# Kernel tuning notes

Measured on AMD Instinct MI355X. Metric: run time of the kernel, lower is better.

## Reference

```python
import jax, jax.numpy as jnp
import numpy as np

D, M, K, L, H, BS = 128, 8, 256, 2, 256, 1024


def setup_inputs() -> dict:
    key = jax.random.key(0)
    ks = jax.random.split(key, 7)
    s_d = 1.0 / np.sqrt(D)
    s_2d = 1.0 / np.sqrt(2 * D)
    s_h = 1.0 / np.sqrt(H)
    x = jax.random.normal(ks[0], (BS, D), jnp.float32)
    codebook0 = jax.random.uniform(ks[1], (K, D), jnp.float32, -s_d, s_d)
    codebooks = jax.random.uniform(ks[2], (M - 1, K, D), jnp.float32, -s_d, s_d)
    Wc = jax.random.uniform(ks[3], (M - 1, D, 2 * D), jnp.float32, -s_2d, s_2d)
    bc = jax.random.uniform(ks[4], (M - 1, D), jnp.float32, -s_2d, s_2d)
    W1 = jax.random.uniform(ks[5], (M - 1, L, H, D), jnp.float32, -s_d, s_d)
    W2 = jax.random.uniform(ks[6], (M - 1, L, D, H), jnp.float32, -s_h, s_h)
    return {"x": x, "codebook0": codebook0, "codebooks": codebooks,
            "Wc": Wc, "bc": bc, "W1": W1, "W2": W2}


def _step_targets(xhat, cb, Wc_m, bc_m, W1_m, W2_m):
    """Candidate quantization targets for one step. xhat:[bs,d], cb:[K,d] -> [bs,K,d].
    MLPconcat(concat(zqs, xhat)) is split into the zqs part and the xhat part so the
    [bs*K, 2d] repeat of the torch code is never materialized (same math)."""
    Wz, Wx = Wc_m[:, :D], Wc_m[:, D:]          # Linear(2d,d): y = cc @ W.T + b
    z = cb[None, :, :] + (cb @ Wz.T)[None, :, :] + (xhat @ Wx.T)[:, None, :] + bc_m  # [bs,K,d]
    for l in range(L):
        z = z + jnp.maximum(jnp.einsum('bkd,hd->bkh', z, W1_m[l]), 0.0) @ W2_m[l].T
    return z + xhat[:, None, :]


def _encode(x, codebook0, codebooks, Wc, bc, W1, W2):
    # step 0: plain nearest-centroid assignment (assign_to_codebook)
    d0 = (x * x).sum(-1, keepdims=True) + (codebook0 * codebook0).sum(-1) - 2.0 * x @ codebook0.T
    code0 = jnp.argmin(d0, axis=1)
    xhat = codebook0[code0]
    codes = [code0]
    xn = (x * x).sum(-1, keepdims=True)        # [bs,1]
    for m in range(M - 1):
        z = _step_targets(xhat, codebooks[m], Wc[m], bc[m], W1[m], W2[m])  # [bs,K,d]
        dist = xn + (z * z).sum(-1) - 2.0 * jnp.einsum('bd,bkd->bk', x, z)
        idx = jnp.argmin(dist, axis=1)
        xhat = jnp.take_along_axis(z, idx[:, None, None], axis=1)[:, 0, :]
        codes.append(idx)
    return jnp.stack(codes, axis=1)            # [bs, M] int


def _decode(codes, codebook0, codebooks, Wc, bc, W1, W2):
    xhat = codebook0[codes[:, 0]]
    side = [xhat]
    for m in range(M - 1):
        zq = codebooks[m][codes[:, m + 1]]     # [bs,d]
        Wz, Wx = Wc[m][:, :D], Wc[m][:, D:]
        z = zq + zq @ Wz.T + xhat @ Wx.T + bc[m]
        for l in range(L):
            z = z + jnp.maximum(z @ W1[m, l].T, 0.0) @ W2[m, l].T
        xhat = xhat + z
        side.append(xhat)
    return xhat, side


def reference(x, codebook0, codebooks, Wc, bc, W1, W2):
    # forward(): encode under no_grad, then differentiable decode with side outputs
    codes = jax.lax.stop_gradient(_encode(x, codebook0, codebooks, Wc, bc, W1, W2))
    xhat, side = _decode(codes, codebook0, codebooks, Wc, bc, W1, W2)
    return (xhat, codes, tuple(side))
```

## Files before the change

kernel.cpp:

```cpp
#include <hip/hip_runtime.h>


typedef _Float16 f16;
typedef f16 half4_t __attribute__((ext_vector_type(4)));
typedef f16 half8_t __attribute__((ext_vector_type(8)));
typedef float f32x16 __attribute__((ext_vector_type(16)));

#define OUT_CODES 131072
#define OUT_SIDE  139264

#define WS_XHAT  0
#define WS_RB    131072
#define WS_Y     262144
#define WS_ZC    393216
#define WS_BESTD 425984
#define WS_BESTI 430080
#define WS_BESTZ 434176
#define WS_WSPLIT 960000
#define NW1 458752

#define HLO 8192

__device__ __forceinline__ f32x16 mfma_f16(half8_t a, half8_t b, f32x16 c) {
  return __builtin_amdgcn_mfma_f32_32x32x16_f16(a, b, c, 0, 0, 0);
}

__global__ __launch_bounds__(256) void k_wsplit(const float* __restrict__ W1,
    const float* __restrict__ W2, f16* __restrict__ wsh)
{
  int i = (blockIdx.x * 256 + threadIdx.x) * 4;
  const float* src;
  f16* hi;
  if (i < NW1) { src = W1 + i; hi = wsh + i; }
  else         { src = W2 + (i - NW1); hi = wsh + 2 * NW1 + (i - NW1); }
  f16* lo = hi + NW1;
  float4 v = *(const float4*)src;
  half4_t h, l;
  float s;
  s = v.x * 256.f; h[0] = (f16)s; l[0] = (f16)(s - (float)h[0]);
  s = v.y * 256.f; h[1] = (f16)s; l[1] = (f16)(s - (float)h[1]);
  s = v.z * 256.f; h[2] = (f16)s; l[2] = (f16)(s - (float)h[2]);
  s = v.w * 256.f; h[3] = (f16)s; l[3] = (f16)(s - (float)h[3]);
  *(half4_t*)hi = h;
  *(half4_t*)lo = l;
}

__global__ __launch_bounds__(256) void k_step0(const float* __restrict__ x,
    const float* __restrict__ cb0, float* __restrict__ ws, float* __restrict__ out)
{
  __shared__ float xs[128];
  __shared__ float redv[4];
  __shared__ int   redi[4];
  __shared__ int   kwin;
  int tx = threadIdx.x, b = blockIdx.x;
  if (tx < 128) xs[tx] = x[b * 128 + tx];
  __syncthreads();
  const float* c = cb0 + tx * 128;
  float s = 0.f;
  for (int d = 0; d < 128; d += 4) {
    float4 cv = *(const float4*)(c + d);
    float4 xv = *(const float4*)(xs + d);
    float a0 = xv.x - cv.x, a1 = xv.y - cv.y, a2 = xv.z - cv.z, a3 = xv.w - cv.w;
    s += a0 * a0 + a1 * a1 + a2 * a2 + a3 * a3;
  }
  float v = s; int idx = tx;
  for (int off = 32; off; off >>= 1) {
    float v2 = __shfl_xor(v, off);
    int   i2 = __shfl_xor(idx, off);
    if (v2 < v || (v2 == v && i2 < idx)) { v = v2; idx = i2; }
  }
  if ((tx & 63) == 0) { redv[tx >> 6] = v; redi[tx >> 6] = idx; }
  __syncthreads();
  if (tx == 0) {
    float bv = redv[0]; int bi = redi[0];
    for (int w = 1; w < 4; w++)
      if (redv[w] < bv || (redv[w] == bv && redi[w] < bi)) { bv = redv[w]; bi = redi[w]; }
    kwin = bi;
    out[OUT_CODES + b * 8] = (float)bi;
  }
  __syncthreads();
  int k = kwin;
  if (tx < 128) {
    float xh = cb0[k * 128 + tx];
    ws[WS_XHAT + b * 128 + tx] = xh;
    ws[WS_RB   + b * 128 + tx] = xs[tx] - xh;
    out[OUT_SIDE + b * 128 + tx] = xh;
  }
}

__global__ __launch_bounds__(128) void k_prep(const float* __restrict__ cb,
    const float* __restrict__ Wc, const float* __restrict__ bcm, float* __restrict__ ws)
{
  __shared__ float row[128];
  int tx = threadIdx.x, blk = blockIdx.x;
  if (blk < 256) {
    row[tx] = cb[blk * 128 + tx];
    __syncthreads();
    const float* wrow = Wc + tx * 256;
    float s = 0.f;
    for (int d = 0; d < 128; d += 4) {
      float4 wv = *(const float4*)(wrow + d);
      float4 zv = *(const float4*)(row + d);
      s += wv.x * zv.x + wv.y * zv.y + wv.z * zv.z + wv.w * zv.w;
    }
    ws[WS_ZC + blk * 128 + tx] = row[tx] + s + bcm[tx];
  } else {
    int b = blk - 256;
    row[tx] = ws[WS_XHAT + b * 128 + tx];
    __syncthreads();
    const float* wrow = Wc + tx * 256 + 128;
    float s = 0.f;
    for (int d = 0; d < 128; d += 4) {
      float4 wv = *(const float4*)(wrow + d);
      float4 zv = *(const float4*)(row + d);
      s += wv.x * zv.x + wv.y * zv.y + wv.z * zv.z + wv.w * zv.w;
    }
    ws[WS_Y + b * 128 + tx] = s;
  }
}

__global__ __launch_bounds__(256, 2) void k_step(const f16* __restrict__ wsh,
    float* __restrict__ ws, int sm)
{
  __shared__ __align__(16) f16 lds[32768];
  f16* Zh = lds;
  f16* Zl = lds + HLO;
  f16* Hh = lds + 2 * HLO;
  f16* Hl = lds + 3 * HLO;
  int tx = threadIdx.x;
  int lane = tx & 63, w = tx >> 6;
  int col = lane & 31, koct = lane >> 5;
  int b = blockIdx.x >> 2, t = blockIdx.x & 3, k0 = t << 6;

  {
    const float* zc = ws + WS_ZC + k0 * 128;
    const float* y  = ws + WS_Y + b * 128;
    for (int idx = tx; idx < 1024; idx += 256) {
      int m = idx & 63, d0 = (idx >> 6) << 3;
      float4 a  = *(const float4*)(zc + m * 128 + d0);
      float4 bb = *(const float4*)(zc + m * 128 + d0 + 4);
      float4 ya = *(const float4*)(y + d0);
      float4 yb = *(const float4*)(y + d0 + 4);
      float sv[8] = {a.x + ya.x, a.y + ya.y, a.z + ya.z, a.w + ya.w,
                     bb.x + yb.x, bb.y + yb.y, bb.z + yb.z, bb.w + yb.w};
      half8_t h8, l8;
#pragma unroll
      for (int j = 0; j < 8; j++) {
        float v = sv[j] * 256.f;
        f16 h = (f16)v; h8[j] = h; l8[j] = (f16)(v - (float)h);
      }
      int c0 = (d0 + ((m & 15) << 3)) & 127;
      *(half8_t*)(Zh + (m << 7) + c0) = h8;
      *(half8_t*)(Zl + (m << 7) + c0) = l8;
    }
  }
  __syncthreads();

  const int rot0 = (col & 15) << 3;
  const f16* Zr0 = Zh + (col << 7);
  const f16* Zr1 = Zh + ((col + 32) << 7);
  const f16* Hr0 = Hh + (col << 7);
  const f16* Hr1 = Hh + ((col + 32) << 7);

  for (int l = 0; l < 2; l++) {
    const f16* w1h = wsh + (size_t)((sm * 2 + l) * 256) * 128;
    const f16* w2h = wsh + 2 * NW1 + (size_t)((sm * 2 + l) * 128) * 256;
    f32x16 acc2[2];
#pragma unroll
    for (int i = 0; i < 16; i++) { acc2[0][i] = 0.f; acc2[1][i] = 0.f; }

#pragma unroll
    for (int hf = 0; hf < 2; hf++) {
      const f16* a1p = w1h + (size_t)((hf << 7) + (w << 5) + col) * 128 + (koct << 3);
      const f16* a2p = w2h + (size_t)((w << 5) + col) * 256 + (hf << 7) + (koct << 3);
      half8_t a1hv[8], a1lv[8], a2hv[8], a2lv[8];
#pragma unroll
      for (int kc = 0; kc < 8; kc++) {
        a1hv[kc] = *(const half8_t*)(a1p + (kc << 4));
        a1lv[kc] = *(const half8_t*)(a1p + NW1 + (kc << 4));
      }
#pragma unroll
      for (int kc = 0; kc < 8; kc++) {
        a2hv[kc] = *(const half8_t*)(a2p + (kc << 4));
        a2lv[kc] = *(const half8_t*)(a2p + NW1 + (kc << 4));
      }

      f32x16 acc1[2];
#pragma unroll
      for (int i = 0; i < 16; i++) { acc1[0][i] = 0.f; acc1[1][i] = 0.f; }
#pragma unroll
      for (int kc = 0; kc < 8; kc++) {
        int poff = (((kc << 4) + (koct << 3)) + rot0) & 127;
        half8_t bh0 = *(const half8_t*)(Zr0 + poff);
        half8_t bl0 = *(const half8_t*)(Zr0 + HLO + poff);
        half8_t bh1 = *(const half8_t*)(Zr1 + poff);
        half8_t bl1 = *(const half8_t*)(Zr1 + HLO + poff);
        acc1[0] = mfma_f16(a1hv[kc], bh0, acc1[0]);
        acc1[1] = mfma_f16(a1hv[kc], bh1, acc1[1]);
        acc1[0] = mfma_f16(a1lv[kc], bh0, acc1[0]);
        acc1[1] = mfma_f16(a1lv[kc], bh1, acc1[1]);
        acc1[0] = mfma_f16(a1hv[kc], bl0, acc1[0]);
        acc1[1] = mfma_f16(a1hv[kc], bl1, acc1[1]);
      }
#pragma unroll
      for (int mt = 0; mt < 2; mt++) {
        int m = (mt << 5) + col;
#pragma unroll
        for (int qd = 0; qd < 4; qd++) {
          half4_t hv, lv;
#pragma unroll
          for (int j = 0; j < 4; j++) {
            float tv = fmaxf(acc1[mt][(qd << 2) + j], 0.f) * 0.00390625f;
            f16 h = (f16)tv; hv[j] = h; lv[j] = (f16)(tv - (float)h);
          }
          int c = (((w << 5) + (qd << 3) + (koct << 2)) + rot0) & 127;
          *(half4_t*)(Hh + (m << 7) + c) = hv;
          *(half4_t*)(Hl + (m << 7) + c) = lv;
        }
      }
      __syncthreads();
#pragma unroll
      for (int kc = 0; kc < 8; kc++) {
        int poff = (((kc << 4) + (koct << 3)) + rot0) & 127;
        half8_t bh0 = *(const half8_t*)(Hr0 + poff);
        half8_t bl0 = *(const half8_t*)(Hr0 + HLO + poff);
        half8_t bh1 = *(const half8_t*)(Hr1 + poff);
        half8_t bl1 = *(const half8_t*)(Hr1 + HLO + poff);
        acc2[0] = mfma_f16(a2hv[kc], bh0, acc2[0]);
        acc2[1] = mfma_f16(a2hv[kc], bh1, acc2[1]);
        acc2[0] = mfma_f16(a2lv[kc], bh0, acc2[0]);
        acc2[1] = mfma_f16(a2lv[kc], bh1, acc2[1]);
        acc2[0] = mfma_f16(a2hv[kc], bl0, acc2[0]);
        acc2[1] = mfma_f16(a2hv[kc], bl1, acc2[1]);
      }
      __syncthreads();
    }
#pragma unroll
    for (int mt = 0; mt < 2; mt++) {
      int m = (mt << 5) + col;
      f16* zhr = Zh + (m << 7);
      f16* zlr = Zl + (m << 7);
#pragma unroll
      for (int qd = 0; qd < 4; qd++) {
        int c = (((w << 5) + (qd << 3) + (koct << 2)) + rot0) & 127;
        half4_t zh = *(half4_t*)(zhr + c);
        half4_t zl = *(half4_t*)(zlr + c);
#pragma unroll
        for (int j = 0; j < 4; j++) {
          float zs = (float)zh[j] + (float)zl[j];
          zs += acc2[mt][(qd << 2) + j] * 0.00390625f;
          f16 h = (f16)zs; zh[j] = h; zl[j] = (f16)(zs - (float)h);
        }
        *(half4_t*)(zhr + c) = zh;
        *(half4_t*)(zlr + c) = zl;
      }
    }
    __syncthreads();
  }

  float* pd = (float*)Hh;
  int* rwin = (int*)Hh + 64;
  {
    int row = tx >> 2, seg = tx & 3;
    int rotr = (row & 15) << 3;
    const f16* zhr = Zh + (row << 7);
    const f16* zlr = Zl + (row << 7);
    const float* rb = ws + WS_RB + b * 128 + (seg << 5);
    float s = 0.f;
#pragma unroll
    for (int o = 0; o < 4; o++) {
      int c = (((seg << 5) + (o << 3)) + rotr) & 127;
      half8_t zh = *(const half8_t*)(zhr + c);
      half8_t zl = *(const half8_t*)(zlr + c);
      float4 r0 = *(const float4*)(rb + (o << 3));
      float4 r1 = *(const float4*)(rb + (o << 3) + 4);
      float rr[8] = {r0.x, r0.y, r0.z, r0.w, r1.x, r1.y, r1.z, r1.w};
#pragma unroll
      for (int j = 0; j < 8; j++) {
        float z = ((float)zh[j] + (float)zl[j]) * 0.00390625f;
        float dlt = rr[j] - z;
        s += dlt * dlt;
      }
    }
    s += __shfl_xor(s, 1);
    s += __shfl_xor(s, 2);
    if (seg == 0) pd[row] = s;
  }
  __syncthreads();
  if (tx < 64) {
    float v = pd[tx]; int idx = tx;
#pragma unroll
    for (int off = 32; off; off >>= 1) {
      float v2 = __shfl_xor(v, off);
      int   i2 = __shfl_xor(idx, off);
      if (v2 < v || (v2 == v && i2 < idx)) { v = v2; idx = i2; }
    }
    if (tx == 0) {
      ws[WS_BESTD + (b << 2) + t] = v;
      ((int*)ws)[WS_BESTI + (b << 2) + t] = k0 + idx;
      rwin[0] = idx;
    }
  }
  __syncthreads();
  if (tx < 32) {
    int rw = rwin[0];
    int c = ((tx << 2) + ((rw & 15) << 3)) & 127;
    half4_t zh = *(const half4_t*)(Zh + (rw << 7) + c);
    half4_t zl = *(const half4_t*)(Zl + (rw << 7) + c);
    float4 z;
    z.x = ((float)zh[0] + (float)zl[0]) * 0.00390625f;
    z.y = ((float)zh[1] + (float)zl[1]) * 0.00390625f;
    z.z = ((float)zh[2] + (float)zl[2]) * 0.00390625f;
    z.w = ((float)zh[3] + (float)zl[3]) * 0.00390625f;
    *(float4*)(ws + WS_BESTZ + (((b << 2) + t) << 7) + (tx << 2)) = z;
  }
}

__global__ __launch_bounds__(128) void k_update(const float* __restrict__ x,
    float* __restrict__ ws, float* __restrict__ out, int m, int last)
{
  __shared__ int tsel;
  int tx = threadIdx.x, b = blockIdx.x;
  if (tx == 0) {
    float bv = ws[WS_BESTD + (b << 2)]; int bt = 0;
    for (int q = 1; q < 4; q++) {
      float v = ws[WS_BESTD + (b << 2) + q];
      if (v < bv) { bv = v; bt = q; }
    }
    tsel = bt;
    int k = ((const int*)ws)[WS_BESTI + (b << 2) + bt];
    out[OUT_CODES + b * 8 + (m + 1)] = (float)k;
  }
  __syncthreads();
  int bt = tsel;
  float z  = ws[WS_BESTZ + (((b << 2) + bt) << 7) + tx];
  float xh = ws[WS_XHAT + b * 128 + tx] + z;
  ws[WS_XHAT + b * 128 + tx] = xh;
  ws[WS_RB   + b * 128 + tx] = x[b * 128 + tx] - xh;
  out[OUT_SIDE + (m + 1) * 131072 + b * 128 + tx] = xh;
  if (last) out[b * 128 + tx] = xh;
}

extern "C" void kernel_launch(void* const* d_in, const int* in_sizes, int n_in,
                              void* d_out, int out_size, void* d_ws, size_t ws_size,
                              hipStream_t stream)
{
  const float* x   = (const float*)d_in[0];
  const float* cb0 = (const float*)d_in[1];
  const float* cbs = (const float*)d_in[2];
  const float* Wc  = (const float*)d_in[3];
  const float* bc  = (const float*)d_in[4];
  const float* W1  = (const float*)d_in[5];
  const float* W2  = (const float*)d_in[6];
  float* out = (float*)d_out;
  float* ws  = (float*)d_ws;
  f16* wsh = (f16*)(ws + WS_WSPLIT);

  k_wsplit<<<896, 256, 0, stream>>>(W1, W2, wsh);
  k_step0<<<1024, 256, 0, stream>>>(x, cb0, ws, out);
  for (int m = 0; m < 7; m++) {
    k_prep<<<1280, 128, 0, stream>>>(cbs + m * 256 * 128, Wc + m * 128 * 256,
                                     bc + m * 128, ws);
    k_step<<<4096, 256, 0, stream>>>(wsh, ws, m);
    k_update<<<1024, 128, 0, stream>>>(x, ws, out, m, (m == 6) ? 1 : 0);
  }
}
```

Baseline: 2.138 ms.

## Retile MFMA warps to 2x2 grid with split-K accumulators for ILP

Changes the per-wave tiling of the two MLP GEMMs in k_step. Each wave now covers one 32-row candidate tile and two 32-column weight tiles, instead of all 64 rows and one weight tile. This halves the LDS B-operand reads per wave and doubles the weight registers held. It also alternates between two accumulator sets over even and odd k-chunks, breaking the MFMA dependency chain, and sums them at the end. The cost is more VGPRs (doubled A fragments and accumulators), which may spill or hurt occupancy under launch_bounds(256,2).

```diff
diff --git a/kernel.cpp b/kernel.cpp
--- a/kernel.cpp
+++ b/kernel.cpp
@@ -130,6 +130,7 @@
   int tx = threadIdx.x;
   int lane = tx & 63, w = tx >> 6;
   int col = lane & 31, koct = lane >> 5;
+  int mb = w & 1, tg = w >> 1;
   int b = blockIdx.x >> 2, t = blockIdx.x & 3, k0 = t << 6;
 
   {
@@ -157,102 +158,106 @@
   __syncthreads();
 
   const int rot0 = (col & 15) << 3;
-  const f16* Zr0 = Zh + (col << 7);
-  const f16* Zr1 = Zh + ((col + 32) << 7);
-  const f16* Hr0 = Hh + (col << 7);
-  const f16* Hr1 = Hh + ((col + 32) << 7);
+  const int mrow = (mb << 5) + col;
+  const f16* Zr = Zh + (mrow << 7);
+  const f16* Hr = Hh + (mrow << 7);
 
   for (int l = 0; l < 2; l++) {
     const f16* w1h = wsh + (size_t)((sm * 2 + l) * 256) * 128;
     const f16* w2h = wsh + 2 * NW1 + (size_t)((sm * 2 + l) * 128) * 256;
-    f32x16 acc2[2];
-#pragma unroll
-    for (int i = 0; i < 16; i++) { acc2[0][i] = 0.f; acc2[1][i] = 0.f; }
+    f32x16 acc2[2][2];
+#pragma unroll
+    for (int i = 0; i < 16; i++) {
+      acc2[0][0][i] = 0.f; acc2[0][1][i] = 0.f;
+      acc2[1][0][i] = 0.f; acc2[1][1][i] = 0.f;
+    }
 
 #pragma unroll
     for (int hf = 0; hf < 2; hf++) {
-      const f16* a1p = w1h + (size_t)((hf << 7) + (w << 5) + col) * 128 + (koct << 3);
-      const f16* a2p = w2h + (size_t)((w << 5) + col) * 256 + (hf << 7) + (koct << 3);
-      half8_t a1hv[8], a1lv[8], a2hv[8], a2lv[8];
+      const f16* a1p = w1h + (size_t)((hf << 7) + (tg << 6) + col) * 128 + (koct << 3);
+      const f16* a2p = w2h + (size_t)((tg << 6) + col) * 256 + (hf << 7) + (koct << 3);
+      half8_t a1h[2][8], a1l[2][8], a2h[2][8], a2l[2][8];
 #pragma unroll
       for (int kc = 0; kc < 8; kc++) {
-        a1hv[kc] = *(const half8_t*)(a1p + (kc << 4));
-        a1lv[kc] = *(const half8_t*)(a1p + NW1 + (kc << 4));
+        a1h[0][kc] = *(const half8_t*)(a1p + (kc << 4));
+        a1l[0][kc] = *(const half8_t*)(a1p + NW1 + (kc << 4));
+        a1h[1][kc] = *(const half8_t*)(a1p + 32 * 128 + (kc << 4));
+        a1l[1][kc] = *(const half8_t*)(a1p + NW1 + 32 * 128 + (kc << 4));
       }
 #pragma unroll
       for (int kc = 0; kc < 8; kc++) {
-        a2hv[kc] = *(const half8_t*)(a2p + (kc << 4));
-        a2lv[kc] = *(const half8_t*)(a2p + NW1 + (kc << 4));
-      }
-
-      f32x16 acc1[2];
-#pragma unroll
-      for (int i = 0; i < 16; i++) { acc1[0][i] = 0.f; acc1[1][i] = 0.f; }
+        a2h[0][kc] = *(const half8_t*)(a2p + (kc << 4));
+        a2l[0][kc] = *(const half8_t*)(a2p + NW1 + (kc << 4));
+        a2h[1][kc] = *(const half8_t*)(a2p + 32 * 256 + (kc << 4));
+        a2l[1][kc] = *(const half8_t*)(a2p + NW1 + 32 * 256 + (kc << 4));
+      }
+
+      f32x16 acc1[2][2];
+#pragma unroll
+      for (int i = 0; i < 16; i++) {
+        acc1[0][0][i] = 0.f; acc1[0][1][i] = 0.f;
+        acc1[1][0][i] = 0.f; acc1[1][1][i] = 0.f;
+      }
 #pragma unroll
       for (int kc = 0; kc < 8; kc++) {
+        int p = kc & 1;
         int poff = (((kc << 4) + (koct << 3)) + rot0) & 127;
-        half8_t bh0 = *(const half8_t*)(Zr0 + poff);
-        half8_t bl0 = *(const half8_t*)(Zr0 + HLO + poff);
-        half8_t bh1 = *(const half8_t*)(Zr1 + poff);
-        half8_t bl1 = *(const half8_t*)(Zr1 + HLO + poff);
-        acc1[0] = mfma_f16(a1hv[kc], bh0, acc1[0]);
-        acc1[1] = mfma_f16(a1hv[kc], bh1, acc1[1]);
-        acc1[0] = mfma_f16(a1lv[kc], bh0, acc1[0]);
-        acc1[1] = mfma_f16(a1lv[kc], bh1, acc1[1]);
-        acc1[0] = mfma_f16(a1hv[kc], bl0, acc1[0]);
-        acc1[1] = mfma_f16(a1hv[kc], bl1, acc1[1]);
-      }
-#pragma unroll
-      for (int mt = 0; mt < 2; mt++) {
-        int m = (mt << 5) + col;
+        half8_t bh = *(const half8_t*)(Zr + poff);
+        half8_t bl = *(const half8_t*)(Zr + HLO + poff);
+        acc1[0][p] = mfma_f16(a1h[0][kc], bh, acc1[0][p]);
+        acc1[1][p] = mfma_f16(a1h[1][kc], bh, acc1[1][p]);
+        acc1[0][p] = mfma_f16(a1l[0][kc], bh, acc1[0][p]);
+        acc1[1][p] = mfma_f16(a1l[1][kc], bh, acc1[1][p]);
+        acc1[0][p] = mfma_f16(a1h[0][kc], bl, acc1[0][p]);
+        acc1[1][p] = mfma_f16(a1h[1][kc], bl, acc1[1][p]);
+      }
+#pragma unroll
+      for (int c = 0; c < 2; c++) {
 #pragma unroll
         for (int qd = 0; qd < 4; qd++) {
           half4_t hv, lv;
 #pragma unroll
           for (int j = 0; j < 4; j++) {
-            float tv = fmaxf(acc1[mt][(qd << 2) + j], 0.f) * 0.00390625f;
+            float tv = fmaxf(acc1[c][0][(qd << 2) + j] + acc1[c][1][(qd << 2) + j], 0.f)
+                       * 0.00390625f;
             f16 h = (f16)tv; hv[j] = h; lv[j] = (f16)(tv - (float)h);
           }
-          int c = (((w << 5) + (qd << 3) + (koct << 2)) + rot0) & 127;
-          *(half4_t*)(Hh + (m << 7) + c) = hv;
-          *(half4_t*)(Hl + (m << 7) + c) = lv;
+          int ca = (((tg << 6) + (c << 5) + (qd << 3) + (koct << 2)) + rot0) & 127;
+          *(half4_t*)(Hh + (mrow << 7) + ca) = hv;
+          *(half4_t*)(Hl + (mrow << 7) + ca) = lv;
         }
       }
       __syncthreads();
 #pragma unroll
       for (int kc = 0; kc < 8; kc++) {
+        int p = kc & 1;
         int poff = (((kc << 4) + (koct << 3)) + rot0) & 127;
-        half8_t bh0 = *(const half8_t*)(Hr0 + poff);
-        half8_t bl0 = *(const half8_t*)(Hr0 + HLO + poff);
-        half8_t bh1 = *(const half8_t*)(Hr1 + poff);
-        half8_t bl1 = *(const half8_t*)(Hr1 + HLO + poff);
-        acc2[0] = mfma_f16(a2hv[kc], bh0, acc2[0]);
-        acc2[1] = mfma_f16(a2hv[kc], bh1, acc2[1]);
-        acc2[0] = mfma_f16(a2lv[kc], bh0, acc2[0]);
-        acc2[1] = mfma_f16(a2lv[kc], bh1, acc2[1]);
-        acc2[0] = mfma_f16(a2hv[kc], bl0, acc2[0]);
-        acc2[1] = mfma_f16(a2hv[kc], bl1, acc2[1]);
+        half8_t bh = *(const half8_t*)(Hr + poff);
+        half8_t bl = *(const half8_t*)(Hr + HLO + poff);
+        acc2[0][p] = mfma_f16(a2h[0][kc], bh, acc2[0][p]);
+        acc2[1][p] = mfma_f16(a2h[1][kc], bh, acc2[1][p]);
+        acc2[0][p] = mfma_f16(a2l[0][kc], bh, acc2[0][p]);
+        acc2[1][p] = mfma_f16(a2l[1][kc], bh, acc2[1][p]);
+        acc2[0][p] = mfma_f16(a2h[0][kc], bl, acc2[0][p]);
+        acc2[1][p] = mfma_f16(a2h[1][kc], bl, acc2[1][p]);
       }
       __syncthreads();
     }
 #pragma unroll
-    for (int mt = 0; mt < 2; mt++) {
-      int m = (mt << 5) + col;
-      f16* zhr = Zh + (m << 7);
-      f16* zlr = Zl + (m << 7);
+    for (int c = 0; c < 2; c++) {
 #pragma unroll
       for (int qd = 0; qd < 4; qd++) {
-        int c = (((w << 5) + (qd << 3) + (koct << 2)) + rot0) & 127;
-        half4_t zh = *(half4_t*)(zhr + c);
-        half4_t zl = *(half4_t*)(zlr + c);
+        int ca = (((tg << 6) + (c << 5) + (qd << 3) + (koct << 2)) + rot0) & 127;
+        half4_t zh = *(half4_t*)(Zh + (mrow << 7) + ca);
+        half4_t zl = *(half4_t*)(Zl + (mrow << 7) + ca);
 #pragma unroll
         for (int j = 0; j < 4; j++) {
           float zs = (float)zh[j] + (float)zl[j];
-          zs += acc2[mt][(qd << 2) + j] * 0.00390625f;
+          zs += (acc2[c][0][(qd << 2) + j] + acc2[c][1][(qd << 2) + j]) * 0.00390625f;
           f16 h = (f16)zs; zh[j] = h; zl[j] = (f16)(zs - (float)h);
         }
-        *(half4_t*)(zhr + c) = zh;
-        *(half4_t*)(zlr + c) = zl;
+        *(half4_t*)(Zh + (mrow << 7) + ca) = zh;
+        *(half4_t*)(Zl + (mrow << 7) + ca) = zl;
       }
     }
     __syncthreads();
```

New measurement: 3.691 ms. +72.7%, slower.

## Repartition k_step warps and stream weight fragments instead of preloading into registers

Applied to the files above, without the earlier changes.

Changes the warp work split in k_step. Each wave now owns one 32-row block of candidates and a 64-wide slice of hidden/output features, where before each wave covered both candidate blocks for a 32-wide slice. The W1/W2 hi/lo fragments are loaded from global memory inside the kc loop rather than preloaded into 32 half8 register arrays. This should cut register pressure and halve LDS B-operand reads per MFMA, at the cost of global weight loads sitting closer to their MFMA uses, which may expose latency.

```diff
diff --git a/kernel.cpp b/kernel.cpp
--- a/kernel.cpp
+++ b/kernel.cpp
@@ -124,12 +124,11 @@
 {
   __shared__ __align__(16) f16 lds[32768];
   f16* Zh = lds;
-  f16* Zl = lds + HLO;
   f16* Hh = lds + 2 * HLO;
-  f16* Hl = lds + 3 * HLO;
   int tx = threadIdx.x;
   int lane = tx & 63, w = tx >> 6;
   int col = lane & 31, koct = lane >> 5;
+  int mb = w & 1, hg = w >> 1;
   int b = blockIdx.x >> 2, t = blockIdx.x & 3, k0 = t << 6;
 
   {
@@ -151,16 +150,15 @@
       }
       int c0 = (d0 + ((m & 15) << 3)) & 127;
       *(half8_t*)(Zh + (m << 7) + c0) = h8;
-      *(half8_t*)(Zl + (m << 7) + c0) = l8;
-    }
-  }
-  __syncthreads();
-
+      *(half8_t*)(Zh + HLO + (m << 7) + c0) = l8;
+    }
+  }
+  __syncthreads();
+
+  const int mrow = (mb << 5) + col;
   const int rot0 = (col & 15) << 3;
-  const f16* Zr0 = Zh + (col << 7);
-  const f16* Zr1 = Zh + ((col + 32) << 7);
-  const f16* Hr0 = Hh + (col << 7);
-  const f16* Hr1 = Hh + ((col + 32) << 7);
+  const f16* Zr = Zh + (mrow << 7);
+  const f16* Hr = Hh + (mrow << 7);
 
   for (int l = 0; l < 2; l++) {
     const f16* w1h = wsh + (size_t)((sm * 2 + l) * 256) * 128;
@@ -171,19 +169,8 @@
 
 #pragma unroll
     for (int hf = 0; hf < 2; hf++) {
-      const f16* a1p = w1h + (size_t)((hf << 7) + (w << 5) + col) * 128 + (koct << 3);
-      const f16* a2p = w2h + (size_t)((w << 5) + col) * 256 + (hf << 7) + (koct << 3);
-      half8_t a1hv[8], a1lv[8], a2hv[8], a2lv[8];
-#pragma unroll
-      for (int kc = 0; kc < 8; kc++) {
-        a1hv[kc] = *(const half8_t*)(a1p + (kc << 4));
-        a1lv[kc] = *(const half8_t*)(a1p + NW1 + (kc << 4));
-      }
-#pragma unroll
-      for (int kc = 0; kc < 8; kc++) {
-        a2hv[kc] = *(const half8_t*)(a2p + (kc << 4));
-        a2lv[kc] = *(const half8_t*)(a2p + NW1 + (kc << 4));
-      }
+      const f16* a1p = w1h + (size_t)((hf << 7) + (hg << 6) + col) * 128 + (koct << 3);
+      const f16* a2p = w2h + (size_t)((hg << 6) + col) * 256 + (hf << 7) + (koct << 3);
 
       f32x16 acc1[2];
 #pragma unroll
@@ -191,68 +178,71 @@
 #pragma unroll
       for (int kc = 0; kc < 8; kc++) {
         int poff = (((kc << 4) + (koct << 3)) + rot0) & 127;
-        half8_t bh0 = *(const half8_t*)(Zr0 + poff);
-        half8_t bl0 = *(const half8_t*)(Zr0 + HLO + poff);
-        half8_t bh1 = *(const half8_t*)(Zr1 + poff);
-        half8_t bl1 = *(const half8_t*)(Zr1 + HLO + poff);
-        acc1[0] = mfma_f16(a1hv[kc], bh0, acc1[0]);
-        acc1[1] = mfma_f16(a1hv[kc], bh1, acc1[1]);
-        acc1[0] = mfma_f16(a1lv[kc], bh0, acc1[0]);
-        acc1[1] = mfma_f16(a1lv[kc], bh1, acc1[1]);
-        acc1[0] = mfma_f16(a1hv[kc], bl0, acc1[0]);
-        acc1[1] = mfma_f16(a1hv[kc], bl1, acc1[1]);
-      }
-#pragma unroll
-      for (int mt = 0; mt < 2; mt++) {
-        int m = (mt << 5) + col;
+        half8_t bh = *(const half8_t*)(Zr + poff);
+        half8_t bl = *(const half8_t*)(Zr + HLO + poff);
+        const f16* a1b = a1p + (kc << 4);
+        half8_t ah0 = *(const half8_t*)(a1b);
+        half8_t ah1 = *(const half8_t*)(a1b + 32 * 128);
+        half8_t al0 = *(const half8_t*)(a1b + NW1);
+        half8_t al1 = *(const half8_t*)(a1b + NW1 + 32 * 128);
+        acc1[0] = mfma_f16(ah0, bh, acc1[0]);
+        acc1[1] = mfma_f16(ah1, bh, acc1[1]);
+        acc1[0] = mfma_f16(al0, bh, acc1[0]);
+        acc1[1] = mfma_f16(al1, bh, acc1[1]);
+        acc1[0] = mfma_f16(ah0, bl, acc1[0]);
+        acc1[1] = mfma_f16(ah1, bl, acc1[1]);
+      }
+#pragma unroll
+      for (int ht = 0; ht < 2; ht++) {
 #pragma unroll
         for (int qd = 0; qd < 4; qd++) {
           half4_t hv, lv;
 #pragma unroll
           for (int j = 0; j < 4; j++) {
-            float tv = fmaxf(acc1[mt][(qd << 2) + j], 0.f) * 0.00390625f;
+            float tv = fmaxf(acc1[ht][(qd << 2) + j], 0.f) * 0.00390625f;
             f16 h = (f16)tv; hv[j] = h; lv[j] = (f16)(tv - (float)h);
           }
-          int c = (((w << 5) + (qd << 3) + (koct << 2)) + rot0) & 127;
-          *(half4_t*)(Hh + (m << 7) + c) = hv;
-          *(half4_t*)(Hl + (m << 7) + c) = lv;
+          int c = (((hg << 6) + (ht << 5) + (qd << 3) + (koct << 2)) + rot0) & 127;
+          *(half4_t*)(Hh + (mrow << 7) + c) = hv;
+          *(half4_t*)(Hh + HLO + (mrow << 7) + c) = lv;
         }
       }
       __syncthreads();
 #pragma unroll
       for (int kc = 0; kc < 8; kc++) {
         int poff = (((kc << 4) + (koct << 3)) + rot0) & 127;
-        half8_t bh0 = *(const half8_t*)(Hr0 + poff);
-        half8_t bl0 = *(const half8_t*)(Hr0 + HLO + poff);
-        half8_t bh1 = *(const half8_t*)(Hr1 + poff);
-        half8_t bl1 = *(const half8_t*)(Hr1 + HLO + poff);
-        acc2[0] = mfma_f16(a2hv[kc], bh0, acc2[0]);
-        acc2[1] = mfma_f16(a2hv[kc], bh1, acc2[1]);
-        acc2[0] = mfma_f16(a2lv[kc], bh0, acc2[0]);
-        acc2[1] = mfma_f16(a2lv[kc], bh1, acc2[1]);
-        acc2[0] = mfma_f16(a2hv[kc], bl0, acc2[0]);
-        acc2[1] = mfma_f16(a2hv[kc], bl1, acc2[1]);
+        half8_t bh = *(const half8_t*)(Hr + poff);
+        half8_t bl = *(const half8_t*)(Hr + HLO + poff);
+        const f16* a2b = a2p + (kc << 4);
+        half8_t ah0 = *(const half8_t*)(a2b);
+        half8_t ah1 = *(const half8_t*)(a2b + 32 * 256);
+        half8_t al0 = *(const half8_t*)(a2b + NW1);
+        half8_t al1 = *(const half8_t*)(a2b + NW1 + 32 * 256);
+        acc2[0] = mfma_f16(ah0, bh, acc2[0]);
+        acc2[1] = mfma_f16(ah1, bh, acc2[1]);
+        acc2[0] = mfma_f16(al0, bh, acc2[0]);
+        acc2[1] = mfma_f16(al1, bh, acc2[1]);
+        acc2[0] = mfma_f16(ah0, bl, acc2[0]);
+        acc2[1] = mfma_f16(ah1, bl, acc2[1]);
       }
       __syncthreads();
     }
 #pragma unroll
-    for (int mt = 0; mt < 2; mt++) {
-      int m = (mt << 5) + col;
-      f16* zhr = Zh + (m << 7);
-      f16* zlr = Zl + (m << 7);
+    for (int dt = 0; dt < 2; dt++) {
+      f16* zhr = Zh + (mrow << 7);
 #pragma unroll
       for (int qd = 0; qd < 4; qd++) {
-        int c = (((w << 5) + (qd << 3) + (koct << 2)) + rot0) & 127;
+        int c = (((hg << 6) + (dt << 5) + (qd << 3) + (koct << 2)) + rot0) & 127;
         half4_t zh = *(half4_t*)(zhr + c);
-        half4_t zl = *(half4_t*)(zlr + c);
+        half4_t zl = *(half4_t*)(zhr + HLO + c);
 #pragma unroll
         for (int j = 0; j < 4; j++) {
           float zs = (float)zh[j] + (float)zl[j];
-          zs += acc2[mt][(qd << 2) + j] * 0.00390625f;
+          zs += acc2[dt][(qd << 2) + j] * 0.00390625f;
           f16 h = (f16)zs; zh[j] = h; zl[j] = (f16)(zs - (float)h);
         }
         *(half4_t*)(zhr + c) = zh;
-        *(half4_t*)(zlr + c) = zl;
+        *(half4_t*)(zhr + HLO + c) = zl;
       }
     }
     __syncthreads();
@@ -264,14 +254,13 @@
     int row = tx >> 2, seg = tx & 3;
     int rotr = (row & 15) << 3;
     const f16* zhr = Zh + (row << 7);
-    const f16* zlr = Zl + (row << 7);
     const float* rb = ws + WS_RB + b * 128 + (seg << 5);
     float s = 0.f;
 #pragma unroll
     for (int o = 0; o < 4; o++) {
       int c = (((seg << 5) + (o << 3)) + rotr) & 127;
       half8_t zh = *(const half8_t*)(zhr + c);
-      half8_t zl = *(const half8_t*)(zlr + c);
+      half8_t zl = *(const half8_t*)(zhr + HLO + c);
       float4 r0 = *(const float4*)(rb + (o << 3));
       float4 r1 = *(const float4*)(rb + (o << 3) + 4);
       float rr[8] = {r0.x, r0.y, r0.z, r0.w, r1.x, r1.y, r1.z, r1.w};
@@ -306,7 +295,7 @@
     int rw = rwin[0];
     int c = ((tx << 2) + ((rw & 15) << 3)) & 127;
     half4_t zh = *(const half4_t*)(Zh + (rw << 7) + c);
-    half4_t zl = *(const half4_t*)(Zl + (rw << 7) + c);
+    half4_t zl = *(const half4_t*)(Zh + HLO + (rw << 7) + c);
     float4 z;
     z.x = ((float)zh[0] + (float)zl[0]) * 0.00390625f;
     z.y = ((float)zh[1] + (float)zl[1]) * 0.00390625f;
```

Result: slower. 3.690 ms (+72.6%).
